# Kernel optimization log

Measured on AMD Instinct MI355X. Metric: run time of the kernel, lower is better.

The kernel has to match this reference:

```python
import jax, jax.numpy as jnp
import numpy as np

B, S, HID = 2, 2048, 2048
NH, NKV, HD = 16, 4, 128  # num_heads, num_kv_heads, head_dim; kqv_size = NH*HD = 2048
KV_DIM = NKV * HD  # 512


def setup_inputs() -> dict:
    key = jax.random.key(0)
    ks = jax.random.split(key, 7)
    sc = 0.02
    return {
        "hidden_states": jax.random.normal(ks[0], (B, S, HID), dtype=jnp.float32),
        "Wq": jax.random.normal(ks[1], (NH * HD, HID), dtype=jnp.float32) * sc,
        "Wk": jax.random.normal(ks[2], (KV_DIM, HID), dtype=jnp.float32) * sc,
        "Wv": jax.random.normal(ks[3], (KV_DIM, HID), dtype=jnp.float32) * sc,
        "Wo": jax.random.normal(ks[4], (HID, NH * HD), dtype=jnp.float32) * sc,
        "bo": jnp.zeros((HID,), dtype=jnp.float32),
    }


def reference(hidden_states, Wq, Wk, Wv, Wo, bo):
    b, s, _ = hidden_states.shape
    # projections (nn.Linear: x @ W.T), no bias on q/k/v
    q = (hidden_states @ Wq.T).reshape(b, s, NH, HD).transpose(0, 2, 1, 3)   # [B,NH,S,HD]
    k = (hidden_states @ Wk.T).reshape(b, s, NKV, HD).transpose(0, 2, 1, 3)  # [B,NKV,S,HD]
    v = (hidden_states @ Wv.T).reshape(b, s, NKV, HD).transpose(0, 2, 1, 3)
    # GQA: query head h uses kv head h // (NH // NKV)
    g = NH // NKV
    k_rep = jnp.repeat(k, g, axis=1)  # [B,NH,S,HD]
    v_rep = jnp.repeat(v, g, axis=1)
    # float32 upcast, NO 1/sqrt(d) scaling (GPT-Neo style)
    qf = q.astype(jnp.float32)
    kf = k_rep.astype(jnp.float32)
    scores = jnp.einsum("bhqd,bhkd->bhqk", qf, kf)  # [B,NH,S,S]
    causal = jnp.tril(jnp.ones((s, s), dtype=bool))[None, None]
    neg = jnp.finfo(scores.dtype).min
    scores = jnp.where(causal, scores, neg)
    attn = jax.nn.softmax(scores, axis=-1).astype(v.dtype)  # dropout p=0 (eval)
    out = jnp.einsum("bhqk,bhkd->bhqd", attn, v_rep)         # [B,NH,S,HD]
    out = out.transpose(0, 2, 1, 3).reshape(b, s, NH * HD)
    return out @ Wo.T + bo
```

## Files before the change

### kernel.cpp

```cpp
#include <hip/hip_runtime.h>

typedef _Float16 f16;
typedef __attribute__((ext_vector_type(4))) _Float16 f16x4;
typedef __attribute__((ext_vector_type(8))) _Float16 f16x8;
typedef __attribute__((ext_vector_type(4))) float f32x4;

#define NB 2
#define NS 2048
#define NHID 2048
#define N_H 16
#define N_KV 4
#define N_HD 128

__device__ __forceinline__ void gload16(void* lds, const void* g) {
  __builtin_amdgcn_global_load_lds(
      (const __attribute__((address_space(1))) unsigned int*)g,
      (__attribute__((address_space(3))) unsigned int*)lds, 16, 0, 0);
}

__global__ __launch_bounds__(256) void cvt_kernel(const float* __restrict__ in,
                                                  f16* __restrict__ out, int n4) {
  int i = blockIdx.x * 256 + threadIdx.x;
  if (i >= n4) return;
  const float4 v = reinterpret_cast<const float4*>(in)[i];
  f16x4 o = {(f16)v.x, (f16)v.y, (f16)v.z, (f16)v.w};
  reinterpret_cast<f16x4*>(out)[i] = o;
}

__global__ __launch_bounds__(256) void cvt3_kernel(const float* __restrict__ a, int na4,
                                                   const float* __restrict__ b, int nb4,
                                                   const float* __restrict__ c, int nc4,
                                                   f16* __restrict__ out) {
  int i = blockIdx.x * 256 + threadIdx.x;
  if (i >= na4 + nb4 + nc4) return;
  const float* src;
  int j;
  if (i < na4) { src = a; j = i; }
  else if (i < na4 + nb4) { src = b; j = i - na4; }
  else { src = c; j = i - na4 - nb4; }
  const float4 v = reinterpret_cast<const float4*>(src)[j];
  f16x4 o = {(f16)v.x, (f16)v.y, (f16)v.z, (f16)v.w};
  reinterpret_cast<f16x4*>(out)[i] = o;
}

template <int MREP, int MODE>
__global__ __launch_bounds__(512, 2) void gemm8(
    const f16* __restrict__ A, const f16* __restrict__ Bm, const int K,
    f16* __restrict__ q_out, f16* __restrict__ k_out, f16* __restrict__ v_out,
    float* __restrict__ f_out, const float* __restrict__ bias) {
  constexpr int BM = MREP * 32;
  constexpr int GA = BM / 128;
  constexpr int G = GA + 2;
  constexpr int NPH = (MREP == 8) ? 2 : 1;
  constexpr int ATILE = BM * 32;
  constexpr int BTILE = 256 * 32;
  constexpr int BUF = ATILE + BTILE;
  __shared__ f16 lds[4 * BUF];

  const int t = threadIdx.x;
  const int l = t & 63, w = t >> 6;
  const int g = l >> 4, l15 = l & 15;
  const int wr = w >> 2, wc = w & 3;
  const int nb = blockIdx.x, mb = blockIdx.y;
  const int NT = K >> 5;

  const f16* Aorig = A + (size_t)(mb * BM) * K;
  const f16* Borig = Bm + (size_t)(nb * 256) * K;

  size_t offA[GA], offB[2];
#pragma unroll
  for (int gi = 0; gi < GA; ++gi) {
    int beta = gi * 8192 + t * 16;
    int r = ((beta >> 9) << 3) | ((beta >> 4) & 7);
    int c = (beta >> 7) & 3;
    offA[gi] = (size_t)r * K + c * 8;
  }
#pragma unroll
  for (int gj = 0; gj < 2; ++gj) {
    int beta = gj * 8192 + t * 16;
    int r = ((beta >> 9) << 3) | ((beta >> 4) & 7);
    int c = (beta >> 7) & 3;
    offB[gj] = (size_t)r * K + c * 8;
  }

  auto stage = [&](int kt, int gi) {
    f16* bufbase = lds + (kt & 3) * BUF;
    if (gi < GA) {
      gload16(bufbase + gi * 4096 + w * 512, Aorig + offA[gi] + kt * 32);
    } else {
      int gj = gi - GA;
      gload16(bufbase + ATILE + gj * 4096 + w * 512, Borig + offB[gj] + kt * 32);
    }
  };
  const int fragoff = ((l15 >> 3) << 8) + (g << 6) + ((l15 & 7) << 3);
  auto readA = [&](int kt, int mi) -> f16x8 {
    int R0 = wr * (MREP * 16) + mi * 16;
    return *reinterpret_cast<const f16x8*>(lds + (kt & 3) * BUF + R0 * 32 + fragoff);
  };
  auto readB = [&](int kt, int ni) -> f16x8 {
    int R0 = wc * 64 + ni * 16;
    return *reinterpret_cast<const f16x8*>(lds + (kt & 3) * BUF + ATILE + R0 * 32 + fragoff);
  };

  f32x4 acc[MREP][4] = {};

#pragma unroll
  for (int pt = 0; pt < 3; ++pt)
#pragma unroll
    for (int gi = 0; gi < G; ++gi) stage(pt, gi);
  if constexpr (MREP == 8) asm volatile("s_waitcnt vmcnt(8)" ::: "memory");
  else                     asm volatile("s_waitcnt vmcnt(6)" ::: "memory");
  __builtin_amdgcn_s_barrier();

  f16x8 bf[4];
  for (int kt = 0; kt < NT; ++kt) {
    const bool dostage = (kt + 3 < NT);
#pragma unroll
    for (int ph = 0; ph < NPH; ++ph) {
      f16x8 af[4];
#pragma unroll
      for (int mi = 0; mi < 4; ++mi) af[mi] = readA(kt, ph * 4 + mi);
      if (ph == 0) {
#pragma unroll
        for (int ni = 0; ni < 4; ++ni) bf[ni] = readB(kt, ni);
      }
      if (dostage) {
        if constexpr (NPH == 2) {
          stage(kt + 3, ph * 2);
          stage(kt + 3, ph * 2 + 1);
        } else {
          stage(kt + 3, 0);
          stage(kt + 3, 1);
          stage(kt + 3, 2);
        }
      }
      if (ph == NPH - 1) {
        if (kt + 3 < NT) {
          if constexpr (MREP == 8) asm volatile("s_waitcnt vmcnt(8)" ::: "memory");
          else                     asm volatile("s_waitcnt vmcnt(6)" ::: "memory");
        } else if (kt + 2 < NT) {
          if constexpr (MREP == 8) asm volatile("s_waitcnt vmcnt(4)" ::: "memory");
          else                     asm volatile("s_waitcnt vmcnt(3)" ::: "memory");
        } else if (kt + 1 < NT) {
          asm volatile("s_waitcnt vmcnt(0)" ::: "memory");
        }
      }
      __builtin_amdgcn_s_barrier();
      asm volatile("s_waitcnt lgkmcnt(0)" ::: "memory");
      __builtin_amdgcn_s_setprio(1);
#pragma unroll
      for (int mi = 0; mi < 4; ++mi)
#pragma unroll
        for (int ni = 0; ni < 4; ++ni)
          acc[ph * 4 + mi][ni] =
              __builtin_amdgcn_mfma_f32_16x16x32_f16(af[mi], bf[ni], acc[ph * 4 + mi][ni], 0, 0, 0);
      __builtin_amdgcn_s_setprio(0);
      __builtin_amdgcn_s_barrier();
    }
  }

#pragma unroll
  for (int mi = 0; mi < MREP; ++mi) {
    int m0 = mb * BM + wr * (MREP * 16) + mi * 16 + 4 * g;
#pragma unroll
    for (int ni = 0; ni < 4; ++ni) {
      int n = nb * 256 + wc * 64 + ni * 16 + l15;
#pragma unroll
      for (int r = 0; r < 4; ++r) {
        int mm = m0 + r;
        float val = acc[mi][ni][r];
        if (MODE == 0) {
          int b = mm >> 11, s = mm & (NS - 1);
          if (n < 2048) {
            int h = n >> 7, d = n & 127;
            q_out[(((size_t)(b * N_H + h)) * NS + s) * N_HD + d] = (f16)val;
          } else if (n < 2560) {
            int n2 = n - 2048, kvh = n2 >> 7, d = n2 & 127;
            k_out[(((size_t)(b * N_KV + kvh)) * NS + s) * N_HD + d] = (f16)val;
          } else {
            int n3 = n - 2560, kvh = n3 >> 7, d = n3 & 127;
            v_out[(((size_t)(b * N_KV + kvh)) * NS + s) * N_HD + d] = (f16)val;
          }
        } else {
          f_out[(size_t)mm * NHID + n] = val + bias[n];
        }
      }
    }
  }
}

__global__ __launch_bounds__(256) void transpose_v(const f16* __restrict__ V,
                                                   f16* __restrict__ Vt) {
  __shared__ f16 tt[64][72];
  int s0 = blockIdx.x * 64, d0 = blockIdx.y * 64, bk = blockIdx.z;
  const f16* Vp = V + (size_t)bk * NS * N_HD;
  f16* Vtp = Vt + (size_t)bk * N_HD * NS;
  int tid = threadIdx.x;
#pragma unroll
  for (int it = 0; it < 2; ++it) {
    int c = it * 256 + tid;
    int sr = c >> 3, dc = (c & 7) * 8;
    f16x8 v = *reinterpret_cast<const f16x8*>(Vp + (size_t)(s0 + sr) * N_HD + d0 + dc);
#pragma unroll
    for (int j = 0; j < 8; ++j) tt[dc + j][sr] = v[j];
  }
  __syncthreads();
#pragma unroll
  for (int it = 0; it < 2; ++it) {
    int c = it * 256 + tid;
    int dr = c >> 3, sc = (c & 7) * 8;
    f16x8 o;
#pragma unroll
    for (int j = 0; j < 8; ++j) o[j] = tt[dr][sc + j];
    *reinterpret_cast<f16x8*>(Vtp + (size_t)(d0 + dr) * NS + s0 + sc) = o;
  }
}

__device__ __forceinline__ void stage_kv(const f16* __restrict__ Kp,
                                         const f16* __restrict__ Vp,
                                         f16* Kl, f16* Vl, int kt, int w, int l) {
#pragma unroll
  for (int it = 0; it < 4; ++it) {
    int cb = (it * 4 + w) * 64;
    int c = cb + l;
    int krow = c >> 4, pch = c & 15;
    int sch = (pch & 8) | ((pch ^ krow) & 7);
    gload16(Kl + cb * 8, Kp + (size_t)(kt * 64 + krow) * N_HD + sch * 8);
  }
#pragma unroll
  for (int it = 0; it < 4; ++it) {
    int cb = (it * 4 + w) * 64;
    int c = cb + l;
    int drow = c >> 3, pch = c & 7;
    int sch = (pch ^ drow) & 7;
    gload16(Vl + cb * 8, Vp + (size_t)drow * NS + kt * 64 + sch * 8);
  }
}

__device__ __forceinline__ void attn_step(
    const f16x8* qf, f32x4* oacc, float* mrow, float* lrow, int q0, int kt,
    const f16* Kl, const f16* Vl, f16* Pw, int g, int l15, bool diag) {
  f32x4 sacc[4];
  __builtin_amdgcn_s_setprio(1);
#pragma unroll
  for (int nt = 0; nt < 4; ++nt) {
    f32x4 z = {0.f, 0.f, 0.f, 0.f};
#pragma unroll
    for (int ks = 0; ks < 4; ++ks) {
      int kr = nt * 16 + l15;
      int ch = ks * 4 + g;
      int sw = (ch & 8) | ((ch ^ kr) & 7);
      f16x8 kf = *reinterpret_cast<const f16x8*>(Kl + kr * 128 + sw * 8);
      z = __builtin_amdgcn_mfma_f32_16x16x32_f16(qf[ks], kf, z, 0, 0, 0);
    }
    sacc[nt] = z;
  }
  __builtin_amdgcn_s_setprio(0);

  float p[4][4], mx[4];
  bool need = false;
#pragma unroll
  for (int r = 0; r < 4; ++r) {
    int qg = q0 + r;
    float m = -3.0e38f;
#pragma unroll
    for (int nt = 0; nt < 4; ++nt) {
      float sv = sacc[nt][r];
      if (diag) {
        int kg = kt * 64 + nt * 16 + l15;
        if (kg > qg) sv = -3.0e38f;
      }
      p[nt][r] = sv;
      m = fmaxf(m, sv);
    }
#pragma unroll
    for (int off = 8; off >= 1; off >>= 1) m = fmaxf(m, __shfl_xor(m, off));
    mx[r] = m;
    need = need || (m > mrow[r] + 11.5f);
  }
  if (__any(need)) {
#pragma unroll
    for (int r = 0; r < 4; ++r) {
      float m2 = fmaxf(mrow[r], mx[r]);
      float alpha = __builtin_amdgcn_exp2f(mrow[r] - m2);
      mrow[r] = m2;
      lrow[r] *= alpha;
#pragma unroll
      for (int dt = 0; dt < 8; ++dt) oacc[dt][r] *= alpha;
    }
  }
#pragma unroll
  for (int r = 0; r < 4; ++r) {
    float rs = 0.f;
#pragma unroll
    for (int nt = 0; nt < 4; ++nt) {
      float pv = __builtin_amdgcn_exp2f(p[nt][r] - mrow[r]);
      p[nt][r] = pv;
      rs += pv;
    }
#pragma unroll
    for (int off = 8; off >= 1; off >>= 1) rs += __shfl_xor(rs, off);
    lrow[r] += rs;
  }

#pragma unroll
  for (int nt = 0; nt < 4; ++nt)
#pragma unroll
    for (int r = 0; r < 4; ++r) {
      int ql = 4 * g + r;
      int kp = nt * 16 + l15;
      int ch = kp >> 3;
      int idx = ql * 64 + (ch ^ (ql & 7)) * 8 + (kp & 7);
      Pw[idx] = (f16)p[nt][r];
    }
  asm volatile("s_waitcnt lgkmcnt(0)" ::: "memory");
  __builtin_amdgcn_sched_barrier(0);

  f16x8 pa[2];
#pragma unroll
  for (int ks2 = 0; ks2 < 2; ++ks2) {
    int ch = ks2 * 4 + g;
    pa[ks2] = *reinterpret_cast<const f16x8*>(&Pw[l15 * 64 + (ch ^ (l15 & 7)) * 8]);
  }
  __builtin_amdgcn_s_setprio(1);
#pragma unroll
  for (int dt = 0; dt < 8; ++dt)
#pragma unroll
    for (int ks2 = 0; ks2 < 2; ++ks2) {
      int d = dt * 16 + l15;
      int ch = ks2 * 4 + g;
      f16x8 vf = *reinterpret_cast<const f16x8*>(Vl + d * 64 + (ch ^ (d & 7)) * 8);
      oacc[dt] = __builtin_amdgcn_mfma_f32_16x16x32_f16(pa[ks2], vf, oacc[dt], 0, 0, 0);
    }
  __builtin_amdgcn_s_setprio(0);
}

__global__ __launch_bounds__(256, 2) void attn_kernel(
    const f16* __restrict__ Q, const f16* __restrict__ K,
    const f16* __restrict__ Vt, f16* __restrict__ O) {
  __shared__ f16 Klds[2][64 * 128];
  __shared__ f16 Vlds[2][128 * 64];
  __shared__ f16 Plds[4][16 * 64];
  const int t = threadIdx.x, l = t & 63, w = t >> 6;
  const int g = l >> 4, l15 = l & 15;
  const int pi = blockIdx.x;
  const int qtA = pi, qtB = 31 - pi;
  const int bh = blockIdx.y;
  const int b = bh >> 4, h = bh & 15;
  const int kvh = h >> 2;
  const f16* Qp = Q + ((size_t)(b * N_H + h)) * NS * N_HD;
  const f16* Kp = K + ((size_t)(b * N_KV + kvh)) * NS * N_HD;
  const f16* Vp = Vt + ((size_t)(b * N_KV + kvh)) * N_HD * NS;

  const f16 l2e = (f16)1.44269504f;
  f16x8 qfA[4], qfB[4];
  const int qrA = qtA * 64 + w * 16 + l15;
  const int qrB = qtB * 64 + w * 16 + l15;
#pragma unroll
  for (int ks = 0; ks < 4; ++ks) {
    qfA[ks] = *reinterpret_cast<const f16x8*>(Qp + (size_t)qrA * N_HD + ks * 32 + g * 8);
    qfB[ks] = *reinterpret_cast<const f16x8*>(Qp + (size_t)qrB * N_HD + ks * 32 + g * 8);
#pragma unroll
    for (int j = 0; j < 8; ++j) { qfA[ks][j] *= l2e; qfB[ks][j] *= l2e; }
  }

  f32x4 oA[8] = {}, oB[8] = {};
  float mA[4], lAr[4], mB[4], lBr[4];
#pragma unroll
  for (int r = 0; r < 4; ++r) {
    mA[r] = -3.0e38f; lAr[r] = 0.f;
    mB[r] = -3.0e38f; lBr[r] = 0.f;
  }
  const int q0A = qtA * 64 + w * 16 + 4 * g;
  const int q0B = qtB * 64 + w * 16 + 4 * g;

  const int nkt = qtB + 1;
  stage_kv(Kp, Vp, Klds[0], Vlds[0], 0, w, l);
  asm volatile("s_waitcnt vmcnt(0)" ::: "memory");
  __syncthreads();
  int cur = 0;
  for (int kt = 0; kt < nkt; ++kt) {
    if (kt + 1 < nkt)
      stage_kv(Kp, Vp, Klds[cur ^ 1], Vlds[cur ^ 1], kt + 1, w, l);
    attn_step(qfB, oB, mB, lBr, q0B, kt, Klds[cur], Vlds[cur], Plds[w], g, l15, kt == qtB);
    if (kt <= qtA)
      attn_step(qfA, oA, mA, lAr, q0A, kt, Klds[cur], Vlds[cur], Plds[w], g, l15, kt == qtA);
    asm volatile("s_waitcnt vmcnt(0)" ::: "memory");
    __syncthreads();
    cur ^= 1;
  }

#pragma unroll
  for (int r = 0; r < 4; ++r) {
    float invB = 1.0f / lBr[r];
    f16* orowB = O + (size_t)(b * NS + q0B + r) * NHID + h * N_HD;
#pragma unroll
    for (int dt = 0; dt < 8; ++dt) orowB[dt * 16 + l15] = (f16)(oB[dt][r] * invB);
    float invA = 1.0f / lAr[r];
    f16* orowA = O + (size_t)(b * NS + q0A + r) * NHID + h * N_HD;
#pragma unroll
    for (int dt = 0; dt < 8; ++dt) orowA[dt * 16 + l15] = (f16)(oA[dt][r] * invA);
  }
}

extern "C" void kernel_launch(void* const* d_in, const int* in_sizes, int n_in,
                              void* d_out, int out_size, void* d_ws, size_t ws_size,
                              hipStream_t stream) {
  const float* hs = (const float*)d_in[0];
  const float* Wq = (const float*)d_in[1];
  const float* Wk = (const float*)d_in[2];
  const float* Wv = (const float*)d_in[3];
  const float* Wo = (const float*)d_in[4];
  const float* bo = (const float*)d_in[5];
  float* out = (float*)d_out;

  char* ws = (char*)d_ws;
  f16* Xh   = (f16*)(ws);
  f16* Wqkv = (f16*)(ws + 16777216);
  f16* Woh  = (f16*)(ws + 29360128);
  f16* Qb   = (f16*)(ws + 37748736);
  f16* Kb   = (f16*)(ws + 54525952);
  f16* Vb   = (f16*)(ws + 58720256);
  f16* Vtb  = (f16*)(ws + 62914560);
  f16* Ob   = Xh;

  cvt_kernel<<<8192, 256, 0, stream>>>(hs, Xh, 2097152);
  cvt3_kernel<<<6144, 256, 0, stream>>>(Wq, 1048576, Wk, 262144, Wv, 262144, Wqkv);
  cvt_kernel<<<4096, 256, 0, stream>>>(Wo, Woh, 1048576);

  gemm8<8, 0><<<dim3(12, 16), 512, 0, stream>>>(Xh, Wqkv, 2048, Qb, Kb, Vb, nullptr, nullptr);
  transpose_v<<<dim3(32, 2, 8), 256, 0, stream>>>(Vb, Vtb);
  attn_kernel<<<dim3(16, 32), 256, 0, stream>>>(Qb, Kb, Vtb, Ob);
  gemm8<4, 1><<<dim3(8, 32), 512, 0, stream>>>(Ob, Woh, 2048, nullptr, nullptr, nullptr, out, bo);
}
```

Before: 239.8 us.

## Interleave dual Q-tile attention MFMAs and remap blocks for XCD-local reuse

Restructures the attention inner loop so the two query tiles (A and B) share each K and V LDS fragment load and interleave their MFMAs, instead of running two separate passes. Each tile gets its own P buffer so both softmax updates can happen before the PV stage. The lazy rescale check is replaced by an unconditional rescale. All three main kernels switch to 1D grids whose block index is remapped so that blocks sharing K/V heads or GEMM tiles land on the same XCD (index modulo 8), improving L2 reuse. The cost is more LDS for the doubled P buffers and higher register pressure.

Result: slower. 255.2 us (+6.4%).

```diff
diff --git a/kernel.cpp b/kernel.cpp
--- a/kernel.cpp
+++ b/kernel.cpp
@@ -61,7 +61,11 @@
   const int l = t & 63, w = t >> 6;
   const int g = l >> 4, l15 = l & 15;
   const int wr = w >> 2, wc = w & 3;
-  const int nb = blockIdx.x, mb = blockIdx.y;
+  const int orig = blockIdx.x;
+  const int x = orig & 7, loc = orig >> 3;
+  int mb, nb;
+  if constexpr (MODE == 0) { mb = (x & 3) * 4 + (loc & 3); nb = (x >> 2) * 6 + (loc >> 2); }
+  else                     { mb = (x & 3) * 8 + (loc & 7); nb = (x >> 2) * 4 + (loc >> 3); }
   const int NT = K >> 5;
 
   const f16* Aorig = A + (size_t)(mb * BM) * K;
@@ -237,11 +241,27 @@
   }
 }
 
-__device__ __forceinline__ void attn_step(
-    const f16x8* qf, f32x4* oacc, float* mrow, float* lrow, int q0, int kt,
-    const f16* Kl, const f16* Vl, f16* Pw, int g, int l15, bool diag) {
-  f32x4 sacc[4];
-  __builtin_amdgcn_s_setprio(1);
+__device__ __forceinline__ void qk_dual(const f16x8* qfA, const f16x8* qfB,
+                                        const f16* Kl, f32x4* sA, f32x4* sB,
+                                        int g, int l15) {
+#pragma unroll
+  for (int nt = 0; nt < 4; ++nt) {
+    f32x4 zA = {0.f, 0.f, 0.f, 0.f}, zB = {0.f, 0.f, 0.f, 0.f};
+#pragma unroll
+    for (int ks = 0; ks < 4; ++ks) {
+      int kr = nt * 16 + l15;
+      int ch = ks * 4 + g;
+      int sw = (ch & 8) | ((ch ^ kr) & 7);
+      f16x8 kf = *reinterpret_cast<const f16x8*>(Kl + kr * 128 + sw * 8);
+      zB = __builtin_amdgcn_mfma_f32_16x16x32_f16(qfB[ks], kf, zB, 0, 0, 0);
+      zA = __builtin_amdgcn_mfma_f32_16x16x32_f16(qfA[ks], kf, zA, 0, 0, 0);
+    }
+    sA[nt] = zA; sB[nt] = zB;
+  }
+}
+
+__device__ __forceinline__ void qk_single(const f16x8* qf, const f16* Kl, f32x4* sB,
+                                          int g, int l15) {
 #pragma unroll
   for (int nt = 0; nt < 4; ++nt) {
     f32x4 z = {0.f, 0.f, 0.f, 0.f};
@@ -253,12 +273,14 @@
       f16x8 kf = *reinterpret_cast<const f16x8*>(Kl + kr * 128 + sw * 8);
       z = __builtin_amdgcn_mfma_f32_16x16x32_f16(qf[ks], kf, z, 0, 0, 0);
     }
-    sacc[nt] = z;
-  }
-  __builtin_amdgcn_s_setprio(0);
-
-  float p[4][4], mx[4];
-  bool need = false;
+    sB[nt] = z;
+  }
+}
+
+__device__ __forceinline__ void sm_update(const f32x4* sacc, float* mrow, float* lrow,
+                                          f32x4* oacc, f16* Pw, int q0, int k0,
+                                          int g, int l15, bool diag) {
+  float p[4][4];
 #pragma unroll
   for (int r = 0; r < 4; ++r) {
     int qg = q0 + r;
@@ -267,7 +289,7 @@
     for (int nt = 0; nt < 4; ++nt) {
       float sv = sacc[nt][r];
       if (diag) {
-        int kg = kt * 64 + nt * 16 + l15;
+        int kg = k0 + nt * 16 + l15;
         if (kg > qg) sv = -3.0e38f;
       }
       p[nt][r] = sv;
@@ -275,34 +297,22 @@
     }
 #pragma unroll
     for (int off = 8; off >= 1; off >>= 1) m = fmaxf(m, __shfl_xor(m, off));
-    mx[r] = m;
-    need = need || (m > mrow[r] + 11.5f);
-  }
-  if (__any(need)) {
-#pragma unroll
-    for (int r = 0; r < 4; ++r) {
-      float m2 = fmaxf(mrow[r], mx[r]);
-      float alpha = __builtin_amdgcn_exp2f(mrow[r] - m2);
-      mrow[r] = m2;
-      lrow[r] *= alpha;
-#pragma unroll
-      for (int dt = 0; dt < 8; ++dt) oacc[dt][r] *= alpha;
-    }
-  }
-#pragma unroll
-  for (int r = 0; r < 4; ++r) {
+    float m2 = fmaxf(mrow[r], m);
+    float alpha = __builtin_amdgcn_exp2f(mrow[r] - m2);
+    mrow[r] = m2;
     float rs = 0.f;
 #pragma unroll
     for (int nt = 0; nt < 4; ++nt) {
-      float pv = __builtin_amdgcn_exp2f(p[nt][r] - mrow[r]);
+      float pv = __builtin_amdgcn_exp2f(p[nt][r] - m2);
       p[nt][r] = pv;
       rs += pv;
     }
 #pragma unroll
     for (int off = 8; off >= 1; off >>= 1) rs += __shfl_xor(rs, off);
-    lrow[r] += rs;
-  }
-
+    lrow[r] = lrow[r] * alpha + rs;
+#pragma unroll
+    for (int dt = 0; dt < 8; ++dt) oacc[dt][r] *= alpha;
+  }
 #pragma unroll
   for (int nt = 0; nt < 4; ++nt)
 #pragma unroll
@@ -313,16 +323,17 @@
       int idx = ql * 64 + (ch ^ (ql & 7)) * 8 + (kp & 7);
       Pw[idx] = (f16)p[nt][r];
     }
-  asm volatile("s_waitcnt lgkmcnt(0)" ::: "memory");
-  __builtin_amdgcn_sched_barrier(0);
-
-  f16x8 pa[2];
+}
+
+__device__ __forceinline__ void pv_dual(const f16* Vl, const f16* PwA, const f16* PwB,
+                                        f32x4* oA, f32x4* oB, int g, int l15) {
+  f16x8 paA[2], paB[2];
 #pragma unroll
   for (int ks2 = 0; ks2 < 2; ++ks2) {
     int ch = ks2 * 4 + g;
-    pa[ks2] = *reinterpret_cast<const f16x8*>(&Pw[l15 * 64 + (ch ^ (l15 & 7)) * 8]);
-  }
-  __builtin_amdgcn_s_setprio(1);
+    paB[ks2] = *reinterpret_cast<const f16x8*>(&PwB[l15 * 64 + (ch ^ (l15 & 7)) * 8]);
+    paA[ks2] = *reinterpret_cast<const f16x8*>(&PwA[l15 * 64 + (ch ^ (l15 & 7)) * 8]);
+  }
 #pragma unroll
   for (int dt = 0; dt < 8; ++dt)
 #pragma unroll
@@ -330,9 +341,28 @@
       int d = dt * 16 + l15;
       int ch = ks2 * 4 + g;
       f16x8 vf = *reinterpret_cast<const f16x8*>(Vl + d * 64 + (ch ^ (d & 7)) * 8);
-      oacc[dt] = __builtin_amdgcn_mfma_f32_16x16x32_f16(pa[ks2], vf, oacc[dt], 0, 0, 0);
-    }
-  __builtin_amdgcn_s_setprio(0);
+      oB[dt] = __builtin_amdgcn_mfma_f32_16x16x32_f16(paB[ks2], vf, oB[dt], 0, 0, 0);
+      oA[dt] = __builtin_amdgcn_mfma_f32_16x16x32_f16(paA[ks2], vf, oA[dt], 0, 0, 0);
+    }
+}
+
+__device__ __forceinline__ void pv_single(const f16* Vl, const f16* PwB,
+                                          f32x4* oB, int g, int l15) {
+  f16x8 pa[2];
+#pragma unroll
+  for (int ks2 = 0; ks2 < 2; ++ks2) {
+    int ch = ks2 * 4 + g;
+    pa[ks2] = *reinterpret_cast<const f16x8*>(&PwB[l15 * 64 + (ch ^ (l15 & 7)) * 8]);
+  }
+#pragma unroll
+  for (int dt = 0; dt < 8; ++dt)
+#pragma unroll
+    for (int ks2 = 0; ks2 < 2; ++ks2) {
+      int d = dt * 16 + l15;
+      int ch = ks2 * 4 + g;
+      f16x8 vf = *reinterpret_cast<const f16x8*>(Vl + d * 64 + (ch ^ (d & 7)) * 8);
+      oB[dt] = __builtin_amdgcn_mfma_f32_16x16x32_f16(pa[ks2], vf, oB[dt], 0, 0, 0);
+    }
 }
 
 __global__ __launch_bounds__(256, 2) void attn_kernel(
@@ -340,14 +370,15 @@
     const f16* __restrict__ Vt, f16* __restrict__ O) {
   __shared__ f16 Klds[2][64 * 128];
   __shared__ f16 Vlds[2][128 * 64];
-  __shared__ f16 Plds[4][16 * 64];
+  __shared__ f16 Plds[4][2][16 * 64];
   const int t = threadIdx.x, l = t & 63, w = t >> 6;
   const int g = l >> 4, l15 = l & 15;
-  const int pi = blockIdx.x;
+  const int orig = blockIdx.x;
+  const int x = orig & 7, loc = orig >> 3;
+  const int b = x >> 2, kvh = x & 3;
+  const int h = kvh * 4 + (loc & 3);
+  const int pi = loc >> 2;
   const int qtA = pi, qtB = 31 - pi;
-  const int bh = blockIdx.y;
-  const int b = bh >> 4, h = bh & 15;
-  const int kvh = h >> 2;
   const f16* Qp = Q + ((size_t)(b * N_H + h)) * NS * N_HD;
   const f16* Kp = K + ((size_t)(b * N_KV + kvh)) * NS * N_HD;
   const f16* Vp = Vt + ((size_t)(b * N_KV + kvh)) * N_HD * NS;
@@ -373,6 +404,8 @@
   }
   const int q0A = qtA * 64 + w * 16 + 4 * g;
   const int q0B = qtB * 64 + w * 16 + 4 * g;
+  f16* PA = &Plds[w][0][0];
+  f16* PB = &Plds[w][1][0];
 
   const int nkt = qtB + 1;
   stage_kv(Kp, Vp, Klds[0], Vlds[0], 0, w, l);
@@ -382,9 +415,21 @@
   for (int kt = 0; kt < nkt; ++kt) {
     if (kt + 1 < nkt)
       stage_kv(Kp, Vp, Klds[cur ^ 1], Vlds[cur ^ 1], kt + 1, w, l);
-    attn_step(qfB, oB, mB, lBr, q0B, kt, Klds[cur], Vlds[cur], Plds[w], g, l15, kt == qtB);
-    if (kt <= qtA)
-      attn_step(qfA, oA, mA, lAr, q0A, kt, Klds[cur], Vlds[cur], Plds[w], g, l15, kt == qtA);
+    const bool doA = (kt <= qtA);
+    f32x4 sA[4], sB[4];
+    __builtin_amdgcn_s_setprio(1);
+    if (doA) qk_dual(qfA, qfB, Klds[cur], sA, sB, g, l15);
+    else     qk_single(qfB, Klds[cur], sB, g, l15);
+    __builtin_amdgcn_s_setprio(0);
+    sm_update(sB, mB, lBr, oB, PB, q0B, kt * 64, g, l15, kt == qtB);
+    if (doA)
+      sm_update(sA, mA, lAr, oA, PA, q0A, kt * 64, g, l15, kt == qtA);
+    asm volatile("s_waitcnt lgkmcnt(0)" ::: "memory");
+    __builtin_amdgcn_sched_barrier(0);
+    __builtin_amdgcn_s_setprio(1);
+    if (doA) pv_dual(Vlds[cur], PA, PB, oA, oB, g, l15);
+    else     pv_single(Vlds[cur], PB, oB, g, l15);
+    __builtin_amdgcn_s_setprio(0);
     asm volatile("s_waitcnt vmcnt(0)" ::: "memory");
     __syncthreads();
     cur ^= 1;
@@ -428,8 +473,8 @@
   cvt3_kernel<<<6144, 256, 0, stream>>>(Wq, 1048576, Wk, 262144, Wv, 262144, Wqkv);
   cvt_kernel<<<4096, 256, 0, stream>>>(Wo, Woh, 1048576);
 
-  gemm8<8, 0><<<dim3(12, 16), 512, 0, stream>>>(Xh, Wqkv, 2048, Qb, Kb, Vb, nullptr, nullptr);
+  gemm8<8, 0><<<192, 512, 0, stream>>>(Xh, Wqkv, 2048, Qb, Kb, Vb, nullptr, nullptr);
   transpose_v<<<dim3(32, 2, 8), 256, 0, stream>>>(Vb, Vtb);
-  attn_kernel<<<dim3(16, 32), 256, 0, stream>>>(Qb, Kb, Vtb, Ob);
-  gemm8<4, 1><<<dim3(8, 32), 512, 0, stream>>>(Ob, Woh, 2048, nullptr, nullptr, nullptr, out, bo);
-}
+  attn_kernel<<<512, 256, 0, stream>>>(Qb, Kb, Vtb, Ob);
+  gemm8<4, 1><<<256, 512, 0, stream>>>(Ob, Woh, 2048, nullptr, nullptr, nullptr, out, bo);
+}
```
